# Optimization experiments

Hardware: AMD Instinct MI355X
Metric: run time of the kernel (lower is better)

## Reference

```python
import jax, jax.numpy as jnp
import numpy as np

N = 65536   # query points
M = 65536   # support points
H = 32      # neighbors per query
IN = 64     # input feature dim
OUT = 64    # out_dim // 2
K = 15      # kernel points
EXTENT = 0.1 * 1.2 / 2.5  # radius * kp_extent / conv_radius = 0.048
BN_EPS = 1e-5


def setup_inputs() -> dict:
    key = jax.random.key(0)
    ks = jax.random.split(key, 8)
    x = jax.random.normal(ks[0], (M, IN), dtype=jnp.float32)
    q_pts = jax.random.uniform(ks[1], (N, 3), dtype=jnp.float32) * 0.1
    s_pts = jax.random.uniform(ks[2], (M, 3), dtype=jnp.float32) * 0.1
    neighb_inds = jax.random.randint(ks[3], (N, H), 0, M, dtype=jnp.int32)
    kernel_points = jax.random.normal(ks[4], (K, 3), dtype=jnp.float32) * (0.5 * EXTENT)
    weights = jax.random.normal(ks[5], (K, IN, OUT), dtype=jnp.float32) * 0.05
    gamma = jnp.ones((OUT,), dtype=jnp.float32)
    beta = jnp.zeros((OUT,), dtype=jnp.float32)
    return {"x": x, "q_pts": q_pts, "s_pts": s_pts, "neighb_inds": neighb_inds,
            "kernel_points": kernel_points, "weights": weights,
            "gamma": gamma, "beta": beta}


def reference(x, q_pts, s_pts, neighb_inds, kernel_points, weights, gamma, beta):
    # --- KPConv (rigid, linear influence, sum aggregation) ---
    # Shadow point/feature for out-of-range neighbor indices (KPConv convention).
    s_pad = jnp.concatenate([s_pts, jnp.full((1, 3), 1e6, s_pts.dtype)], axis=0)
    x_pad = jnp.concatenate([x, jnp.zeros((1, x.shape[1]), x.dtype)], axis=0)

    # Relative neighbor coordinates: [N, H, 3]
    neighbors = s_pad[neighb_inds] - q_pts[:, None, :]
    # Squared distance to each kernel point: [N, H, K]
    diffs = neighbors[:, :, None, :] - kernel_points[None, None, :, :]
    sq_dist = jnp.sum(diffs * diffs, axis=-1)
    # Linear kernel-point influence, clipped at 0: [N, H, K]
    all_weights = jnp.maximum(1.0 - jnp.sqrt(sq_dist) / EXTENT, 0.0)

    # Gather neighbor features: [N, H, IN]
    neighb_x = x_pad[neighb_inds]
    # Influence-weighted aggregation per kernel point: [N, K, IN]
    weighted = jnp.einsum('nhk,nhi->nki', all_weights, neighb_x)
    # Apply per-kernel-point weight matrices and sum over kernel points: [N, OUT]
    out = jnp.einsum('nki,kio->no', weighted, weights)

    # --- BatchNorm (training-mode statistics over points) ---
    mean = jnp.mean(out, axis=0)
    var = jnp.var(out, axis=0)
    out = (out - mean) / jnp.sqrt(var + BN_EPS) * gamma + beta

    # --- LeakyReLU(0.1) ---
    return jnp.where(out >= 0, out, 0.1 * out)
```

## Files before the change

### kernel.cpp

```cpp
#include <hip/hip_runtime.h>
#include <math.h>

#define NQ   65536
#define H    32
#define IN   64
#define OUTC 64
#define K    15
#define QB   16
#define S_XN 68
#define S_WT 36
#define AK   72
#define AROW 1076
#define INV_EXT (1.0f / 0.048f)

#define OFF_PSUM  131072
#define OFF_SCSH  (OFF_PSUM + 2097152)
#define OFF_XBF   (OFF_SCSH + 1024)
#define NEED_BF16 (OFF_XBF + (size_t)NQ * IN * 2)

typedef __attribute__((ext_vector_type(8))) short short8;
typedef __attribute__((ext_vector_type(4))) short short4v;
typedef __attribute__((ext_vector_type(4))) float float4v;

static __device__ __forceinline__ unsigned short f2bf(float f) {
    return (unsigned short)((__float_as_uint(f) + 0x8000u) >> 16);
}
static __device__ __forceinline__ unsigned pk2(float a, float b) {
    return (__float_as_uint(a) + 0x8000u) >> 16 |
           ((__float_as_uint(b) + 0x8000u) & 0xFFFF0000u);
}

__global__ __launch_bounds__(256) void prep_all(
    const float* __restrict__ W, const float* __restrict__ x,
    short* __restrict__ Bfrag, unsigned short* __restrict__ xbf, int do_x)
{
    const int b = blockIdx.x;
    if (b < 4096) {
        if (do_x) {
            const int t = b * 256 + threadIdx.x;
            const float4 v = ((const float4*)x)[t];
            uint2 p; p.x = pk2(v.x, v.y); p.y = pk2(v.z, v.w);
            ((uint2*)xbf)[t] = p;
        }
    } else {
        const int t2 = (b - 4096) * 256 + threadIdx.x;
        const int o  = t2 & 63;
        const int i  = (t2 >> 6) & 63;
        const int kq = t2 >> 12;
        const int t  = kq * 2 + (i >> 5);
        const int lane = ((i >> 3) & 3) * 16 + (o & 15);
        const int v  = o >> 4;
        const int j  = i & 7;
        Bfrag[((v * 30 + t) * 64 + lane) * 8 + j] = (short)f2bf(W[t2]);
    }
}

template<bool BFX>
__global__ __launch_bounds__(256, 4) void kpconv_mfma(
    const float* __restrict__ x, const unsigned short* __restrict__ xbf,
    const float* __restrict__ qp, const float* __restrict__ sp,
    const int* __restrict__ inds, const float* __restrict__ kp,
    const short* __restrict__ Bfrag, float* __restrict__ out_raw,
    float* __restrict__ psum)
{
    __shared__ __align__(16) short lds[17920];
    short* xn  = lds;
    short* wT  = lds + 8704;
    short* Awt = lds;

    const int tid  = threadIdx.x;
    const int lane = tid & 63;
    const int wv   = tid >> 6;
    const int quad = lane >> 4;
    const int ml   = lane & 15;
    const int q0   = blockIdx.x * QB;

    for (int rep = 0; rep < 2; ++rep) {
        const int pair = tid + rep * 256;
        const int q = pair >> 5, h = pair & 31;
        const int n = q0 + q;
        const int id = inds[n * H + h];
        const float dx = sp[id * 3 + 0] - qp[n * 3 + 0];
        const float dy = sp[id * 3 + 1] - qp[n * 3 + 1];
        const float dz = sp[id * 3 + 2] - qp[n * 3 + 2];
#pragma unroll
        for (int k = 0; k < K; ++k) {
            const float ex = dx - kp[k * 3 + 0];
            const float ey = dy - kp[k * 3 + 1];
            const float ez = dz - kp[k * 3 + 2];
            const float sq = ex * ex + ey * ey + ez * ez;
            float wval = 1.0f - __builtin_amdgcn_sqrtf(sq) * INV_EXT;
            wval = wval > 0.0f ? wval : 0.0f;
            wT[(q * 16 + k) * S_WT + h] = (short)f2bf(wval);
        }
        wT[(q * 16 + K) * S_WT + h] = 0;
    }
    __syncthreads();

    float4v frag[QB];
#pragma unroll
    for (int qg = 0; qg < QB; ++qg) frag[qg] = (float4v){0.f, 0.f, 0.f, 0.f};

    for (int b = 0; b < 4; ++b) {
        const int qg_s = 4 * b + wv;
        const int ibase = (q0 + qg_s) * H;
#pragma unroll
        for (int j = 0; j < 8; ++j) {
            const int h = j * 4 + quad;
            const int id = inds[ibase + h];
            if (BFX) {
                const short4v xv = *(const short4v*)((const short*)xbf + id * IN + ml * 4);
                *(short4v*)&xn[(wv * H + h) * S_XN + ml * 4] = xv;
            } else {
                const float4 xv = *(const float4*)(x + id * IN + ml * 4);
                short4v p;
                p[0] = (short)f2bf(xv.x); p[1] = (short)f2bf(xv.y);
                p[2] = (short)f2bf(xv.z); p[3] = (short)f2bf(xv.w);
                *(short4v*)&xn[(wv * H + h) * S_XN + ml * 4] = p;
            }
        }
        __syncthreads();
#pragma unroll
        for (int ql = 0; ql < 4; ++ql) {
            const int qg = 4 * b + ql;
            const int arow = (qg * 16 + ml) * S_WT + quad * 8;
            const short4v alo = *(const short4v*)&wT[arow];
            const short4v ahi = *(const short4v*)&wT[arow + 4];
            short8 a;
#pragma unroll
            for (int e = 0; e < 4; ++e) { a[e] = alo[e]; a[e + 4] = ahi[e]; }
            short8 bb;
#pragma unroll
            for (int j = 0; j < 8; ++j)
                bb[j] = xn[(ql * H + quad * 8 + j) * S_XN + wv * 16 + ml];
            frag[qg] = __builtin_amdgcn_mfma_f32_16x16x32_bf16(a, bb, frag[qg], 0, 0, 0);
        }
        __syncthreads();
    }

#pragma unroll
    for (int qg = 0; qg < QB; ++qg) {
#pragma unroll
        for (int r = 0; r < 4; ++r) {
            const int kq = quad * 4 + r;
            if (kq < K)
                Awt[qg * AROW + kq * AK + wv * 16 + ml] = (short)f2bf(frag[qg][r]);
        }
    }
    __syncthreads();

    float4v acc = (float4v){0.f, 0.f, 0.f, 0.f};
    const short* bptr = Bfrag + (wv * 30) * 512 + lane * 8;
#pragma unroll 2
    for (int t = 0; t < 30; ++t) {
        const int abase = ml * AROW + (t >> 1) * AK + (t & 1) * 32 + quad * 8;
        const short4v alo = *(const short4v*)&Awt[abase];
        const short4v ahi = *(const short4v*)&Awt[abase + 4];
        short8 a;
#pragma unroll
        for (int e = 0; e < 4; ++e) { a[e] = alo[e]; a[e + 4] = ahi[e]; }
        const short8 bb = *(const short8*)(bptr + t * 512);
        acc = __builtin_amdgcn_mfma_f32_16x16x32_bf16(a, bb, acc, 0, 0, 0);
    }

    float s = 0.f, s2 = 0.f;
#pragma unroll
    for (int r = 0; r < 4; ++r) {
        const float v = acc[r];
        out_raw[(q0 + quad * 4 + r) * OUTC + wv * 16 + ml] = v;
        s += v; s2 += v * v;
    }
    s  += __shfl_xor(s, 16, 64);  s  += __shfl_xor(s, 32, 64);
    s2 += __shfl_xor(s2, 16, 64); s2 += __shfl_xor(s2, 32, 64);
    if (quad == 0) {
        const int c = wv * 16 + ml;
        psum[c * 4096 + blockIdx.x]          = s;
        psum[262144 + c * 4096 + blockIdx.x] = s2;
    }
}

__global__ __launch_bounds__(256) void bn_stats(
    const float* __restrict__ psum, const float* __restrict__ gamma,
    const float* __restrict__ beta, float* __restrict__ sc_sh)
{
    const int c = blockIdx.x;
    const int t = threadIdx.x;
    float s = 0.f, q = 0.f;
#pragma unroll
    for (int i = 0; i < 16; ++i) {
        s += psum[c * 4096 + t + i * 256];
        q += psum[262144 + c * 4096 + t + i * 256];
    }
    __shared__ float rs[4], rq[4];
#pragma unroll
    for (int off = 32; off; off >>= 1) {
        s += __shfl_down(s, off, 64);
        q += __shfl_down(q, off, 64);
    }
    if ((t & 63) == 0) { rs[t >> 6] = s; rq[t >> 6] = q; }
    __syncthreads();
    if (t == 0) {
        s = rs[0] + rs[1] + rs[2] + rs[3];
        q = rq[0] + rq[1] + rq[2] + rq[3];
        const float mean = s * (1.0f / (float)NQ);
        const float var  = q * (1.0f / (float)NQ) - mean * mean;
        const float scale = gamma[c] / sqrtf(var + 1e-5f);
        sc_sh[c]      = scale;
        sc_sh[64 + c] = beta[c] - mean * scale;
    }
}

__global__ __launch_bounds__(256) void bn_apply(
    float* __restrict__ out, const float* __restrict__ sc_sh)
{
    __shared__ float sc[64];
    __shared__ float sh[64];
    if (threadIdx.x < 64) {
        sc[threadIdx.x] = sc_sh[threadIdx.x];
        sh[threadIdx.x] = sc_sh[64 + threadIdx.x];
    }
    __syncthreads();
    const int idx = blockIdx.x * 256 + threadIdx.x;
#pragma unroll
    for (int it = 0; it < 4; ++it) {
        const int e = idx + it * 262144;
        float4 v = ((const float4*)out)[e];
        const int cg = (e & 15) * 4;
        float4 r;
        r.x = v.x * sc[cg + 0] + sh[cg + 0];
        r.y = v.y * sc[cg + 1] + sh[cg + 1];
        r.z = v.z * sc[cg + 2] + sh[cg + 2];
        r.w = v.w * sc[cg + 3] + sh[cg + 3];
        r.x = r.x >= 0.0f ? r.x : 0.1f * r.x;
        r.y = r.y >= 0.0f ? r.y : 0.1f * r.y;
        r.z = r.z >= 0.0f ? r.z : 0.1f * r.z;
        r.w = r.w >= 0.0f ? r.w : 0.1f * r.w;
        ((float4*)out)[e] = r;
    }
}

extern "C" void kernel_launch(void* const* d_in, const int* in_sizes, int n_in,
                              void* d_out, int out_size, void* d_ws, size_t ws_size,
                              hipStream_t stream)
{
    (void)in_sizes; (void)n_in; (void)out_size;
    const float* x     = (const float*)d_in[0];
    const float* qp    = (const float*)d_in[1];
    const float* sp    = (const float*)d_in[2];
    const int*   inds  = (const int*)d_in[3];
    const float* kp    = (const float*)d_in[4];
    const float* W     = (const float*)d_in[5];
    const float* gamma = (const float*)d_in[6];
    const float* beta  = (const float*)d_in[7];
    float* out = (float*)d_out;

    short*          Bfrag = (short*)d_ws;
    float*          psum  = (float*)((char*)d_ws + OFF_PSUM);
    float*          sc_sh = (float*)((char*)d_ws + OFF_SCSH);
    unsigned short* xbf   = (unsigned short*)((char*)d_ws + OFF_XBF);

    const int use_bf = (ws_size >= NEED_BF16) ? 1 : 0;

    prep_all<<<4336, 256, 0, stream>>>(W, x, Bfrag, xbf, use_bf);
    if (use_bf)
        kpconv_mfma<true><<<NQ / QB, 256, 0, stream>>>(x, xbf, qp, sp, inds, kp, Bfrag, out, psum);
    else
        kpconv_mfma<false><<<NQ / QB, 256, 0, stream>>>(x, xbf, qp, sp, inds, kp, Bfrag, out, psum);
    bn_stats<<<64, 256, 0, stream>>>(psum, gamma, beta, sc_sh);
    bn_apply<<<1024, 256, 0, stream>>>(out, sc_sh);
}
```

Baseline: 162.0 us.

## Interleave influence compute with gathers, shrink LDS, and fuse BN stats into apply

The influence-weight computation is now done per 4-query batch inside the gather loop, with each lane pair handling one neighbor. Gathered features are loaded into registers first so their latency overlaps the weight math. The smaller wT buffer and reduced AK/AROW padding cut LDS per block, and launch bounds rise to 5 blocks per CU. BN partial sums now go through atomics into 64 slots zeroed in the prep kernel, and the separate stats kernel is folded into bn_apply, which removes one launch. The costs are atomic contention, every bn_apply block re-reducing the stats, and possible register spills under the tighter occupancy bound.

```diff
diff --git a/kernel.cpp b/kernel.cpp
--- a/kernel.cpp
+++ b/kernel.cpp
@@ -9,13 +9,12 @@
 #define QB   16
 #define S_XN 68
 #define S_WT 36
-#define AK   72
-#define AROW 1076
+#define AK   68
+#define AROW 1020
 #define INV_EXT (1.0f / 0.048f)
 
 #define OFF_PSUM  131072
-#define OFF_SCSH  (OFF_PSUM + 2097152)
-#define OFF_XBF   (OFF_SCSH + 1024)
+#define OFF_XBF   163840
 #define NEED_BF16 (OFF_XBF + (size_t)NQ * IN * 2)
 
 typedef __attribute__((ext_vector_type(8))) short short8;
@@ -32,7 +31,8 @@
 
 __global__ __launch_bounds__(256) void prep_all(
     const float* __restrict__ W, const float* __restrict__ x,
-    short* __restrict__ Bfrag, unsigned short* __restrict__ xbf, int do_x)
+    short* __restrict__ Bfrag, unsigned short* __restrict__ xbf,
+    float* __restrict__ psum2, int do_x)
 {
     const int b = blockIdx.x;
     if (b < 4096) {
@@ -42,7 +42,7 @@
             uint2 p; p.x = pk2(v.x, v.y); p.y = pk2(v.z, v.w);
             ((uint2*)xbf)[t] = p;
         }
-    } else {
+    } else if (b < 4336) {
         const int t2 = (b - 4096) * 256 + threadIdx.x;
         const int o  = t2 & 63;
         const int i  = (t2 >> 6) & 63;
@@ -52,18 +52,23 @@
         const int v  = o >> 4;
         const int j  = i & 7;
         Bfrag[((v * 30 + t) * 64 + lane) * 8 + j] = (short)f2bf(W[t2]);
+    } else {
+        float4 z = {0.f, 0.f, 0.f, 0.f};
+#pragma unroll
+        for (int i = 0; i < 8; ++i)
+            ((float4*)psum2)[threadIdx.x + 256 * i] = z;
     }
 }
 
 template<bool BFX>
-__global__ __launch_bounds__(256, 4) void kpconv_mfma(
+__global__ __launch_bounds__(256, 5) void kpconv_mfma(
     const float* __restrict__ x, const unsigned short* __restrict__ xbf,
     const float* __restrict__ qp, const float* __restrict__ sp,
     const int* __restrict__ inds, const float* __restrict__ kp,
     const short* __restrict__ Bfrag, float* __restrict__ out_raw,
-    float* __restrict__ psum)
-{
-    __shared__ __align__(16) short lds[17920];
+    float* __restrict__ psum2)
+{
+    __shared__ __align__(16) short lds[16320];
     short* xn  = lds;
     short* wT  = lds + 8704;
     short* Awt = lds;
@@ -75,55 +80,63 @@
     const int ml   = lane & 15;
     const int q0   = blockIdx.x * QB;
 
-    for (int rep = 0; rep < 2; ++rep) {
-        const int pair = tid + rep * 256;
-        const int q = pair >> 5, h = pair & 31;
-        const int n = q0 + q;
-        const int id = inds[n * H + h];
-        const float dx = sp[id * 3 + 0] - qp[n * 3 + 0];
-        const float dy = sp[id * 3 + 1] - qp[n * 3 + 1];
-        const float dz = sp[id * 3 + 2] - qp[n * 3 + 2];
-#pragma unroll
-        for (int k = 0; k < K; ++k) {
-            const float ex = dx - kp[k * 3 + 0];
-            const float ey = dy - kp[k * 3 + 1];
-            const float ez = dz - kp[k * 3 + 2];
-            const float sq = ex * ex + ey * ey + ez * ez;
-            float wval = 1.0f - __builtin_amdgcn_sqrtf(sq) * INV_EXT;
-            wval = wval > 0.0f ? wval : 0.0f;
-            wT[(q * 16 + k) * S_WT + h] = (short)f2bf(wval);
-        }
-        wT[(q * 16 + K) * S_WT + h] = 0;
-    }
-    __syncthreads();
-
     float4v frag[QB];
 #pragma unroll
     for (int qg = 0; qg < QB; ++qg) frag[qg] = (float4v){0.f, 0.f, 0.f, 0.f};
 
     for (int b = 0; b < 4; ++b) {
-        const int qg_s = 4 * b + wv;
-        const int ibase = (q0 + qg_s) * H;
+        const int ibase = (q0 + 4 * b + wv) * H;
+        short4v xv[8];
+        float4  xf[8];
 #pragma unroll
         for (int j = 0; j < 8; ++j) {
-            const int h = j * 4 + quad;
-            const int id = inds[ibase + h];
+            const int id = inds[ibase + j * 4 + quad];
+            if (BFX)
+                xv[j] = *(const short4v*)((const short*)xbf + id * IN + ml * 4);
+            else
+                xf[j] = *(const float4*)(x + id * IN + ml * 4);
+        }
+
+        {
+            const int h = lane >> 1, half = lane & 1;
+            const int nq_ = q0 + 4 * b + wv;
+            const int idA = inds[nq_ * H + h];
+            const float dx = sp[idA * 3 + 0] - qp[nq_ * 3 + 0];
+            const float dy = sp[idA * 3 + 1] - qp[nq_ * 3 + 1];
+            const float dz = sp[idA * 3 + 2] - qp[nq_ * 3 + 2];
+#pragma unroll
+            for (int kk = 0; kk < 8; ++kk) {
+                const int k = half * 8 + kk;
+                float wval = 0.f;
+                if (k < K) {
+                    const float ex = dx - kp[k * 3 + 0];
+                    const float ey = dy - kp[k * 3 + 1];
+                    const float ez = dz - kp[k * 3 + 2];
+                    const float sq = ex * ex + ey * ey + ez * ez;
+                    wval = 1.0f - __builtin_amdgcn_sqrtf(sq) * INV_EXT;
+                    wval = wval > 0.0f ? wval : 0.0f;
+                }
+                wT[(wv * 16 + k) * S_WT + h] = (short)f2bf(wval);
+            }
+        }
+
+#pragma unroll
+        for (int j = 0; j < 8; ++j) {
             if (BFX) {
-                const short4v xv = *(const short4v*)((const short*)xbf + id * IN + ml * 4);
-                *(short4v*)&xn[(wv * H + h) * S_XN + ml * 4] = xv;
+                *(short4v*)&xn[(wv * H + j * 4 + quad) * S_XN + ml * 4] = xv[j];
             } else {
-                const float4 xv = *(const float4*)(x + id * IN + ml * 4);
                 short4v p;
-                p[0] = (short)f2bf(xv.x); p[1] = (short)f2bf(xv.y);
-                p[2] = (short)f2bf(xv.z); p[3] = (short)f2bf(xv.w);
-                *(short4v*)&xn[(wv * H + h) * S_XN + ml * 4] = p;
+                p[0] = (short)f2bf(xf[j].x); p[1] = (short)f2bf(xf[j].y);
+                p[2] = (short)f2bf(xf[j].z); p[3] = (short)f2bf(xf[j].w);
+                *(short4v*)&xn[(wv * H + j * 4 + quad) * S_XN + ml * 4] = p;
             }
         }
         __syncthreads();
+
 #pragma unroll
         for (int ql = 0; ql < 4; ++ql) {
             const int qg = 4 * b + ql;
-            const int arow = (qg * 16 + ml) * S_WT + quad * 8;
+            const int arow = (ql * 16 + ml) * S_WT + quad * 8;
             const short4v alo = *(const short4v*)&wT[arow];
             const short4v ahi = *(const short4v*)&wT[arow + 4];
             short8 a;
@@ -174,50 +187,37 @@
     s2 += __shfl_xor(s2, 16, 64); s2 += __shfl_xor(s2, 32, 64);
     if (quad == 0) {
         const int c = wv * 16 + ml;
-        psum[c * 4096 + blockIdx.x]          = s;
-        psum[262144 + c * 4096 + blockIdx.x] = s2;
-    }
-}
-
-__global__ __launch_bounds__(256) void bn_stats(
-    const float* __restrict__ psum, const float* __restrict__ gamma,
-    const float* __restrict__ beta, float* __restrict__ sc_sh)
-{
-    const int c = blockIdx.x;
-    const int t = threadIdx.x;
-    float s = 0.f, q = 0.f;
+        const int slot = blockIdx.x & 63;
+        atomicAdd(&psum2[slot * 64 + c], s);
+        atomicAdd(&psum2[4096 + slot * 64 + c], s2);
+    }
+}
+
+__global__ __launch_bounds__(256) void bn_apply(
+    float* __restrict__ out, const float* __restrict__ psum2,
+    const float* __restrict__ gamma, const float* __restrict__ beta)
+{
+    __shared__ float red[8][64];
+    __shared__ float sc[64], sh[64];
+    const int c = threadIdx.x & 63;
+    const int g = threadIdx.x >> 6;
+    float s = 0.f, q2 = 0.f;
 #pragma unroll
     for (int i = 0; i < 16; ++i) {
-        s += psum[c * 4096 + t + i * 256];
-        q += psum[262144 + c * 4096 + t + i * 256];
-    }
-    __shared__ float rs[4], rq[4];
-#pragma unroll
-    for (int off = 32; off; off >>= 1) {
-        s += __shfl_down(s, off, 64);
-        q += __shfl_down(q, off, 64);
-    }
-    if ((t & 63) == 0) { rs[t >> 6] = s; rq[t >> 6] = q; }
+        const int sl = g * 16 + i;
+        s  += psum2[sl * 64 + c];
+        q2 += psum2[4096 + sl * 64 + c];
+    }
+    red[g][c] = s; red[4 + g][c] = q2;
     __syncthreads();
-    if (t == 0) {
-        s = rs[0] + rs[1] + rs[2] + rs[3];
-        q = rq[0] + rq[1] + rq[2] + rq[3];
+    if (g == 0) {
+        s  = red[0][c] + red[1][c] + red[2][c] + red[3][c];
+        q2 = red[4][c] + red[5][c] + red[6][c] + red[7][c];
         const float mean = s * (1.0f / (float)NQ);
-        const float var  = q * (1.0f / (float)NQ) - mean * mean;
+        const float var  = q2 * (1.0f / (float)NQ) - mean * mean;
         const float scale = gamma[c] / sqrtf(var + 1e-5f);
-        sc_sh[c]      = scale;
-        sc_sh[64 + c] = beta[c] - mean * scale;
-    }
-}
-
-__global__ __launch_bounds__(256) void bn_apply(
-    float* __restrict__ out, const float* __restrict__ sc_sh)
-{
-    __shared__ float sc[64];
-    __shared__ float sh[64];
-    if (threadIdx.x < 64) {
-        sc[threadIdx.x] = sc_sh[threadIdx.x];
-        sh[threadIdx.x] = sc_sh[64 + threadIdx.x];
+        sc[c] = scale;
+        sh[c] = beta[c] - mean * scale;
     }
     __syncthreads();
     const int idx = blockIdx.x * 256 + threadIdx.x;
@@ -255,17 +255,15 @@
     float* out = (float*)d_out;
 
     short*          Bfrag = (short*)d_ws;
-    float*          psum  = (float*)((char*)d_ws + OFF_PSUM);
-    float*          sc_sh = (float*)((char*)d_ws + OFF_SCSH);
+    float*          psum2 = (float*)((char*)d_ws + OFF_PSUM);
     unsigned short* xbf   = (unsigned short*)((char*)d_ws + OFF_XBF);
 
     const int use_bf = (ws_size >= NEED_BF16) ? 1 : 0;
 
-    prep_all<<<4336, 256, 0, stream>>>(W, x, Bfrag, xbf, use_bf);
+    prep_all<<<4337, 256, 0, stream>>>(W, x, Bfrag, xbf, psum2, use_bf);
     if (use_bf)
-        kpconv_mfma<true><<<NQ / QB, 256, 0, stream>>>(x, xbf, qp, sp, inds, kp, Bfrag, out, psum);
+        kpconv_mfma<true><<<NQ / QB, 256, 0, stream>>>(x, xbf, qp, sp, inds, kp, Bfrag, out, psum2);
     else
-        kpconv_mfma<false><<<NQ / QB, 256, 0, stream>>>(x, xbf, qp, sp, inds, kp, Bfrag, out, psum);
-    bn_stats<<<64, 256, 0, stream>>>(psum, gamma, beta, sc_sh);
-    bn_apply<<<1024, 256, 0, stream>>>(out, sc_sh);
-}
+        kpconv_mfma<false><<<NQ / QB, 256, 0, stream>>>(x, xbf, qp, sp, inds, kp, Bfrag, out, psum2);
+    bn_apply<<<1024, 256, 0, stream>>>(out, psum2, gamma, beta);
+}
```

Measured after the change: 198.3 us. 1.22x slower.
